# Kernel tuning notes

Hardware: AMD Instinct MI355X
Metric: run time of the kernel (lower is better)

The kernel has to match this reference:

```python
import jax, jax.numpy as jnp
import numpy as np

D = 256      # input channels
DK = 64      # key/query/value channels
BS, W, H = 8, 64, 64


def setup_inputs() -> dict:
    key = jax.random.key(0)
    k1, k2, k3, k4 = jax.random.split(key, 4)
    v = jax.random.normal(k1, (BS, D, W, H), dtype=jnp.float32)
    # conv1x1 weights collapse to plain matrices over the channel dim
    Wqkv = jax.random.normal(k2, (3 * DK, D), dtype=jnp.float32) * 0.02
    Wout = jax.random.normal(k3, (D, DK), dtype=jnp.float32) * 0.02
    gamma = jax.random.normal(k4, (1,), dtype=jnp.float32)  # original inits to 0; nonzero for a non-degenerate baseline
    return {"v": v, "Wqkv": Wqkv, "Wout": Wout, "gamma": gamma}


def reference(v, Wqkv, Wout, gamma):
    bs, c, w, h = v.shape
    n = w * h
    d_k = Wout.shape[1]
    x = v.reshape(bs, c, n)                      # (b, c, n)
    qkv = jnp.einsum('oc,bcn->bon', Wqkv, x)      # 1x1 conv == channel matmul
    q = qkv[:, :d_k]                              # (b, dk, n)
    k = qkv[:, d_k:2 * d_k]
    val = qkv[:, 2 * d_k:]
    s = jnp.einsum('bdi,bdj->bij', q, k)          # (b, n, n) = query^T key
    beta = jax.nn.softmax(s, axis=2)              # exp(s - logsumexp(s, axis=2))
    y = jnp.einsum('bdi,bij->bdj', val, beta)     # bmm(value, beta)
    o = jnp.einsum('od,bdn->bon', Wout, y) * gamma[0] + x
    return o.reshape(bs, c, w, h)
```

## Files before the change

### kernel.cpp

```cpp
#include <hip/hip_runtime.h>

typedef unsigned short ushort_t;
typedef __bf16 bf16x8 __attribute__((ext_vector_type(8)));
typedef short short4v __attribute__((ext_vector_type(4)));
typedef float f32x4 __attribute__((ext_vector_type(4)));
typedef unsigned int uint4v __attribute__((ext_vector_type(4)));
typedef unsigned int uint2v __attribute__((ext_vector_type(2)));

#define NTOK 4096
#define DMODEL 256
#define DK 64
#define BS 8
#define LN2INV 1.44269504088896f

__device__ __forceinline__ ushort_t f2bf(float f) {
  unsigned u = __builtin_bit_cast(unsigned, f);
  u += 0x7fffu + ((u >> 16) & 1u);
  return (ushort_t)(u >> 16);
}
__device__ __forceinline__ float bf2f(ushort_t s) {
  return __builtin_bit_cast(float, ((unsigned)s) << 16);
}
__device__ __forceinline__ bf16x8 lds_frag(const ushort_t* p) {
  return __builtin_bit_cast(bf16x8, *(const uint4v*)p);
}
__device__ __forceinline__ bf16x8 ldg8(const ushort_t* p) {
  return __builtin_bit_cast(bf16x8, *(const uint4v*)p);
}
__device__ __forceinline__ short4v lo8(uint4v v) {
  uint2v t; t.x = v.x; t.y = v.y;
  return __builtin_bit_cast(short4v, t);
}
__device__ __forceinline__ short4v hi8(uint4v v) {
  uint2v t; t.x = v.z; t.y = v.w;
  return __builtin_bit_cast(short4v, t);
}
__device__ __forceinline__ float fexp2(float x) {
#if __has_builtin(__builtin_amdgcn_exp2f)
  return __builtin_amdgcn_exp2f(x);
#else
  return exp2f(x);
#endif
}
__device__ __forceinline__ unsigned bfpack(float x, float y) {
  return __builtin_amdgcn_perm(__builtin_bit_cast(unsigned, y),
                               __builtin_bit_cast(unsigned, x), 0x07060302u);
}
__device__ __forceinline__ f32x4 mfma16(short4v a, short4v b, f32x4 c) {
#if defined(__HIP_DEVICE_COMPILE__)
#if __has_builtin(__builtin_amdgcn_mfma_f32_16x16x16bf16_1k)
  return __builtin_amdgcn_mfma_f32_16x16x16bf16_1k(a, b, c, 0, 0, 0);
#else
  typedef __bf16 bf16x4 __attribute__((ext_vector_type(4)));
  return __builtin_amdgcn_mfma_f32_16x16x16_bf16(__builtin_bit_cast(bf16x4, a),
                                                 __builtin_bit_cast(bf16x4, b), c, 0, 0, 0);
#endif
#else
  (void)a; (void)b;
  return c;
#endif
}

__global__ __launch_bounds__(256) void k_convert(const float* __restrict__ Wqkv,
                                                 const float* __restrict__ Wout,
                                                 ushort_t* __restrict__ Wb,
                                                 ushort_t* __restrict__ Woutb) {
  int i = blockIdx.x * 256 + threadIdx.x;
  if (i < 3 * DK * DMODEL) {
    float w = Wqkv[i];
    if (i < DK * DMODEL) w *= LN2INV;
    Wb[i] = f2bf(w);
  } else {
    int j = i - 3 * DK * DMODEL;
    Woutb[j] = f2bf(Wout[j]);
  }
}

__global__ __launch_bounds__(256) void k_qkv(const float* __restrict__ x,
                                             const ushort_t* __restrict__ W,
                                             ushort_t* __restrict__ QT,
                                             ushort_t* __restrict__ KT,
                                             ushort_t* __restrict__ Vf) {
  const int b = blockIdx.y;
  const int n0 = blockIdx.x * 64;
  const int tid = threadIdx.x;
  const int lane = tid & 63, wv = tid >> 6;
  const int quad = lane >> 4, l15 = lane & 15;
  __shared__ __align__(16) ushort_t lx[64 * 264];
  __shared__ __align__(16) ushort_t t[64 * 72];

  const float* xb = x + (size_t)b * DMODEL * NTOK;

#pragma unroll 1
  for (int cc = 0; cc < 4; cc++) {
    const int c0chunk = cc * 64;
#pragma unroll
    for (int kr = 0; kr < 2; kr++) {
      int s = tid + 256 * kr;
      int c = s >> 3, ns = (s & 7) * 8;
      const float* src = xb + (size_t)(c0chunk + c) * NTOK + n0 + ns;
      f32x4 a = *(const f32x4*)src;
      f32x4 bq = *(const f32x4*)(src + 4);
      uint4v o;
      o.x = (unsigned)f2bf(a[0]) | ((unsigned)f2bf(a[1]) << 16);
      o.y = (unsigned)f2bf(a[2]) | ((unsigned)f2bf(a[3]) << 16);
      o.z = (unsigned)f2bf(bq[0]) | ((unsigned)f2bf(bq[1]) << 16);
      o.w = (unsigned)f2bf(bq[2]) | ((unsigned)f2bf(bq[3]) << 16);
      *(uint4v*)(t + c * 72 + ns) = o;
    }
    __syncthreads();
#pragma unroll
    for (int kr = 0; kr < 2; kr++) {
      int s = tid + 256 * kr;
      int n = s >> 3, cs = (s & 7) * 8;
      unsigned e0 = t[(cs + 0) * 72 + n], e1 = t[(cs + 1) * 72 + n];
      unsigned e2 = t[(cs + 2) * 72 + n], e3 = t[(cs + 3) * 72 + n];
      unsigned e4 = t[(cs + 4) * 72 + n], e5 = t[(cs + 5) * 72 + n];
      unsigned e6 = t[(cs + 6) * 72 + n], e7 = t[(cs + 7) * 72 + n];
      uint4v o;
      o.x = e0 | (e1 << 16); o.y = e2 | (e3 << 16);
      o.z = e4 | (e5 << 16); o.w = e6 | (e7 << 16);
      *(uint4v*)(lx + n * 264 + c0chunk + cs) = o;
    }
    __syncthreads();
  }

  f32x4 acc[3][4];
  const f32x4 zero4 = {0.f, 0.f, 0.f, 0.f};
#pragma unroll
  for (int i = 0; i < 3; i++)
#pragma unroll
    for (int j = 0; j < 4; j++) acc[i][j] = zero4;

#pragma unroll
  for (int c0 = 0; c0 < DMODEL; c0 += 32) {
    bf16x8 aw[3];
#pragma unroll
    for (int mt = 0; mt < 3; mt++)
      aw[mt] = ldg8(W + (wv * 48 + mt * 16 + l15) * DMODEL + c0 + quad * 8);
    bf16x8 bb[4];
#pragma unroll
    for (int nt = 0; nt < 4; nt++)
      bb[nt] = lds_frag(lx + (nt * 16 + l15) * 264 + c0 + quad * 8);
#pragma unroll
    for (int mt = 0; mt < 3; mt++)
#pragma unroll
      for (int nt = 0; nt < 4; nt++)
        acc[mt][nt] = __builtin_amdgcn_mfma_f32_16x16x32_bf16(aw[mt], bb[nt], acc[mt][nt], 0, 0, 0);
  }

#pragma unroll
  for (int mt = 0; mt < 3; mt++) {
    int o = wv * 48 + mt * 16 + quad * 4;
#pragma unroll
    for (int nt = 0; nt < 4; nt++) {
      int n = n0 + nt * 16 + l15;
      f32x4 v4 = acc[mt][nt];
      if (o < 128) {
        ushort_t* dst = (o < 64) ? (QT + ((size_t)b * NTOK + n) * DK + o)
                                 : (KT + ((size_t)b * NTOK + n) * DK + (o - 64));
        uint2v ww;
        ww.x = (unsigned)f2bf(v4[0]) | ((unsigned)f2bf(v4[1]) << 16);
        ww.y = (unsigned)f2bf(v4[2]) | ((unsigned)f2bf(v4[3]) << 16);
        *(uint2v*)dst = ww;
      } else {
        int dbase = o - 128;
        size_t tbase = ((((size_t)b * 64 + (n0 >> 6)) * 4 + nt) * 2 + (dbase >> 5)) * 512;
        ushort_t* vp = Vf + tbase + ((l15 >> 2) << 7) + ((dbase & 15) << 3) +
                       (((dbase >> 4) & 1) << 2) + (l15 & 3);
#pragma unroll
        for (int r = 0; r < 4; r++) vp[r << 3] = f2bf(v4[r]);
      }
    }
  }
}

__global__ __launch_bounds__(512, 4) void k_rsum(const ushort_t* __restrict__ QT,
                                                 const ushort_t* __restrict__ KT,
                                                 float* __restrict__ Rr) {
  const int id = blockIdx.x;
  const int b = id & 7;
  const int i0 = (id >> 3) * 64;
  const int tid = threadIdx.x;
  const int lane = tid & 63, wv = tid >> 6;
  const int quad = lane >> 4, l15 = lane & 15;
  __shared__ __align__(16) float partial[8 * 64];
  const ushort_t* QTb = QT + ((size_t)b * NTOK + i0) * DK;
  const ushort_t* KTb = KT + ((size_t)b * NTOK + wv * 512) * DK;

  bf16x8 aq0[4], aq1[4];
#pragma unroll
  for (int isub = 0; isub < 4; isub++) {
    const ushort_t* qp = QTb + (size_t)(isub * 16 + l15) * DK + quad * 8;
    aq0[isub] = ldg8(qp);
    aq1[isub] = ldg8(qp + 32);
  }

  f32x4 racc[4];
  const f32x4 zero4 = {0.f, 0.f, 0.f, 0.f};
#pragma unroll
  for (int isub = 0; isub < 4; isub++) racc[isub] = zero4;

#pragma unroll 1
  for (int ph = 0; ph < 8; ph++) {
    const ushort_t* kb_base = KTb + (size_t)ph * 64 * DK;
    bf16x8 kb0[4], kb1[4];
#pragma unroll
    for (int nt = 0; nt < 4; nt++) {
      const ushort_t* kp = kb_base + (size_t)(nt * 16 + l15) * DK + quad * 8;
      kb0[nt] = ldg8(kp);
      kb1[nt] = ldg8(kp + 32);
    }
#pragma unroll
    for (int isub = 0; isub < 4; isub++)
#pragma unroll
      for (int nt = 0; nt < 4; nt++) {
        f32x4 s4 = __builtin_amdgcn_mfma_f32_16x16x32_bf16(aq0[isub], kb0[nt], zero4, 0, 0, 0);
        s4 = __builtin_amdgcn_mfma_f32_16x16x32_bf16(aq1[isub], kb1[nt], s4, 0, 0, 0);
        racc[isub][0] += fexp2(s4[0]);
        racc[isub][1] += fexp2(s4[1]);
        racc[isub][2] += fexp2(s4[2]);
        racc[isub][3] += fexp2(s4[3]);
      }
  }

#pragma unroll
  for (int isub = 0; isub < 4; isub++)
#pragma unroll
    for (int r = 0; r < 4; r++) {
      float v = racc[isub][r];
      v += __shfl_xor(v, 1);
      v += __shfl_xor(v, 2);
      v += __shfl_xor(v, 4);
      v += __shfl_xor(v, 8);
      racc[isub][r] = v;
    }
  if (l15 == 0) {
#pragma unroll
    for (int isub = 0; isub < 4; isub++)
      *(f32x4*)(partial + wv * 64 + isub * 16 + quad * 4) = racc[isub];
  }
  __syncthreads();
  if (tid < 64) {
    float s = 0.f;
#pragma unroll
    for (int w = 0; w < 8; w++) s += partial[w * 64 + tid];
    Rr[(size_t)b * NTOK + i0 + tid] = -__log2f(s);
  }
}

__global__ __launch_bounds__(256, 4) void k_pv(const ushort_t* __restrict__ QT,
                                               const ushort_t* __restrict__ KT,
                                               const ushort_t* __restrict__ Vf,
                                               const float* __restrict__ Rr,
                                               ushort_t* __restrict__ Yp) {
  const int id = blockIdx.x;
  const int b = id & 7;
  const int rest = id >> 3;
  const int j0 = (rest & 63) * 64;
  const int ih = rest >> 6;
  const int tid = threadIdx.x;
  const int lane = tid & 63, wv = tid >> 6;
  const int quad = lane >> 4, l15 = lane & 15;

  __shared__ __align__(16) ushort_t pool[13312];
  float* rbuf = (float*)pool;
  ushort_t* pbuf = pool + 8704;

  const ushort_t* KTb = KT + ((size_t)b * NTOK + j0) * DK;
  const ushort_t* QTb = QT + ((size_t)b * NTOK + ih * 2048) * DK;
  const ushort_t* Vfb = Vf + ((size_t)b * 64 + ih * 32) * 4096;
  const float* Rrb = Rr + (size_t)b * NTOK + ih * 2048;

  bf16x8 kb0[4], kb1[4];
#pragma unroll
  for (int nt = 0; nt < 4; nt++) {
    const ushort_t* kp = KTb + (size_t)(nt * 16 + l15) * DK + quad * 8;
    kb0[nt] = ldg8(kp);
    kb1[nt] = ldg8(kp + 32);
  }

  f32x4 yt[4][4];
  const f32x4 zero4 = {0.f, 0.f, 0.f, 0.f};
#pragma unroll
  for (int i = 0; i < 4; i++)
#pragma unroll
    for (int j = 0; j < 4; j++) yt[i][j] = zero4;

  const int qrow = (wv * 16 + l15) * DK + quad * 8;
  const int vfo = wv * 1024 + lane * 8;

#pragma unroll 1
  for (int it = 0; it < 32; it++) {
    const ushort_t* qp = QTb + (size_t)it * 64 * DK + qrow;
    bf16x8 a0 = ldg8(qp);
    bf16x8 a1 = ldg8(qp + 32);
    const ushort_t* vp = Vfb + (size_t)it * 4096 + vfo;
    uint4v vv0 = *(const uint4v*)vp;
    uint4v vv1 = *(const uint4v*)(vp + 512);
    f32x4 lrv = *(const f32x4*)(Rrb + it * 64 + wv * 16 + quad * 4);
    short4v vf0 = lo8(vv0), vf1 = hi8(vv0), vf2 = lo8(vv1), vf3 = hi8(vv1);
#pragma unroll
    for (int nt = 0; nt < 4; nt++) {
      f32x4 s4 = __builtin_amdgcn_mfma_f32_16x16x32_bf16(a0, kb0[nt], lrv, 0, 0, 0);
      s4 = __builtin_amdgcn_mfma_f32_16x16x32_bf16(a1, kb1[nt], s4, 0, 0, 0);
      uint2v wp;
      wp.x = bfpack(fexp2(s4[0]), fexp2(s4[1]));
      wp.y = bfpack(fexp2(s4[2]), fexp2(s4[3]));
      short4v wf = __builtin_bit_cast(short4v, wp);
      yt[nt][0] = mfma16(wf, vf0, yt[nt][0]);
      yt[nt][1] = mfma16(wf, vf1, yt[nt][1]);
      yt[nt][2] = mfma16(wf, vf2, yt[nt][2]);
      yt[nt][3] = mfma16(wf, vf3, yt[nt][3]);
    }
  }

  if (wv == 0) {
#pragma unroll
    for (int nt = 0; nt < 4; nt++)
#pragma unroll
      for (int dsub = 0; dsub < 4; dsub++)
        *(f32x4*)(rbuf + (dsub * 16 + l15) * 68 + nt * 16 + quad * 4) = yt[nt][dsub];
  }
  __syncthreads();
  if (wv == 1) {
#pragma unroll
    for (int nt = 0; nt < 4; nt++)
#pragma unroll
      for (int dsub = 0; dsub < 4; dsub++) {
        float* p = rbuf + (dsub * 16 + l15) * 68 + nt * 16 + quad * 4;
        *(f32x4*)p = *(const f32x4*)p + yt[nt][dsub];
      }
  }
  __syncthreads();
  if (wv == 2) {
#pragma unroll
    for (int nt = 0; nt < 4; nt++)
#pragma unroll
      for (int dsub = 0; dsub < 4; dsub++) {
        float* p = rbuf + (dsub * 16 + l15) * 68 + nt * 16 + quad * 4;
        *(f32x4*)p = *(const f32x4*)p + yt[nt][dsub];
      }
  }
  __syncthreads();
  if (wv == 3) {
#pragma unroll
    for (int nt = 0; nt < 4; nt++)
#pragma unroll
      for (int dsub = 0; dsub < 4; dsub++) {
        const float* p = rbuf + (dsub * 16 + l15) * 68 + nt * 16 + quad * 4;
        f32x4 v4 = *(const f32x4*)p + yt[nt][dsub];
#pragma unroll
        for (int r = 0; r < 4; r++)
          pbuf[(nt * 16 + quad * 4 + r) * 72 + dsub * 16 + l15] = f2bf(v4[r]);
      }
  }
  __syncthreads();

  ushort_t* Ypb = Yp + ((size_t)(ih * 8 + b) * NTOK + j0) * DK;
#pragma unroll
  for (int kr = 0; kr < 2; kr++) {
    int s = tid + 256 * kr;
    int row = s >> 3, cc = (s & 7) * 8;
    *(uint4v*)(Ypb + (size_t)row * DK + cc) = *(const uint4v*)(pbuf + row * 72 + cc);
  }
}

__global__ __launch_bounds__(256) void k_out(const ushort_t* __restrict__ Yp,
                                             const ushort_t* __restrict__ Wout,
                                             const float* __restrict__ gammap,
                                             const float* __restrict__ x,
                                             float* __restrict__ outp) {
  const int id = blockIdx.x;
  const int b = id & 7;
  const int n0 = (id >> 3) * 64;
  const int tid = threadIdx.x;
  const int lane = tid & 63, wv = tid >> 6;
  const int quad = lane >> 4, l15 = lane & 15;
  __shared__ __align__(16) ushort_t pbuf[64 * 72];

  const ushort_t* Y0 = Yp + ((size_t)b * NTOK + n0) * DK;
  const ushort_t* Y1 = Yp + ((size_t)(8 + b) * NTOK + n0) * DK;
#pragma unroll
  for (int kr = 0; kr < 2; kr++) {
    int s = tid + 256 * kr;
    int row = s >> 3, c8 = (s & 7) * 8;
    uint4v ua = *(const uint4v*)(Y0 + (size_t)row * DK + c8);
    uint4v ub = *(const uint4v*)(Y1 + (size_t)row * DK + c8);
    uint4v oc;
    unsigned* pa = (unsigned*)&ua;
    unsigned* pb = (unsigned*)&ub;
    unsigned* po = (unsigned*)&oc;
#pragma unroll
    for (int w = 0; w < 4; w++) {
      float lo = bf2f((ushort_t)(pa[w] & 0xffff)) + bf2f((ushort_t)(pb[w] & 0xffff));
      float hi = bf2f((ushort_t)(pa[w] >> 16)) + bf2f((ushort_t)(pb[w] >> 16));
      po[w] = bfpack(lo, hi);
    }
    *(uint4v*)(pbuf + row * 72 + c8) = oc;
  }
  __syncthreads();

  const f32x4 zero4 = {0.f, 0.f, 0.f, 0.f};
  bf16x8 yb0[4], yb1[4];
#pragma unroll
  for (int nt = 0; nt < 4; nt++) {
    yb0[nt] = lds_frag(pbuf + (nt * 16 + l15) * 72 + quad * 8);
    yb1[nt] = lds_frag(pbuf + (nt * 16 + l15) * 72 + 32 + quad * 8);
  }
  f32x4 oacc[4][4];
#pragma unroll
  for (int m = 0; m < 4; m++)
#pragma unroll
    for (int nt = 0; nt < 4; nt++) oacc[m][nt] = zero4;
#pragma unroll
  for (int m = 0; m < 4; m++) {
    int c = (wv * 4 + m) * 16 + l15;
    bf16x8 aw0 = __builtin_bit_cast(bf16x8, *(const uint4v*)(Wout + c * DK + quad * 8));
    bf16x8 aw1 = __builtin_bit_cast(bf16x8, *(const uint4v*)(Wout + c * DK + 32 + quad * 8));
#pragma unroll
    for (int nt = 0; nt < 4; nt++) {
      oacc[m][nt] = __builtin_amdgcn_mfma_f32_16x16x32_bf16(aw0, yb0[nt], oacc[m][nt], 0, 0, 0);
      oacc[m][nt] = __builtin_amdgcn_mfma_f32_16x16x32_bf16(aw1, yb1[nt], oacc[m][nt], 0, 0, 0);
    }
  }
  float g = gammap[0];
  const float* xb = x + (size_t)b * DMODEL * NTOK;
  float* ob = outp + (size_t)b * DMODEL * NTOK;
#pragma unroll
  for (int m = 0; m < 4; m++) {
    int cbase = (wv * 4 + m) * 16 + quad * 4;
#pragma unroll
    for (int nt = 0; nt < 4; nt++) {
      int n = n0 + nt * 16 + l15;
#pragma unroll
      for (int r = 0; r < 4; r++) {
        size_t idx = (size_t)(cbase + r) * NTOK + n;
        ob[idx] = oacc[m][nt][r] * g + xb[idx];
      }
    }
  }
}

extern "C" void kernel_launch(void* const* d_in, const int* in_sizes, int n_in,
                              void* d_out, int out_size, void* d_ws, size_t ws_size,
                              hipStream_t stream) {
  const float* v = (const float*)d_in[0];
  const float* Wqkv = (const float*)d_in[1];
  const float* Wout = (const float*)d_in[2];
  const float* gamma = (const float*)d_in[3];
  float* outp = (float*)d_out;

  ushort_t* QT = (ushort_t*)d_ws;
  ushort_t* KT = QT + (size_t)BS * NTOK * DK;
  ushort_t* Vf = KT + (size_t)BS * NTOK * DK;
  ushort_t* Wb = Vf + (size_t)BS * DK * NTOK;
  ushort_t* Woutb = Wb + 3 * DK * DMODEL;
  float* Rr = (float*)(Woutb + DMODEL * DK);
  ushort_t* Yp = (ushort_t*)(Rr + (size_t)BS * NTOK);

  k_convert<<<dim3(256), 256, 0, stream>>>(Wqkv, Wout, Wb, Woutb);
  k_qkv<<<dim3(64, BS), 256, 0, stream>>>(v, Wb, QT, KT, Vf);
  k_rsum<<<dim3(512), 512, 0, stream>>>(QT, KT, Rr);
  k_pv<<<dim3(1024), 256, 0, stream>>>(QT, KT, Vf, Rr, Yp);
  k_out<<<dim3(512), 256, 0, stream>>>(Yp, Woutb, gamma, v, outp);
}
```

Measured before the change: 203.9 us.

## Double-buffer Q and V tiles in k_pv via async global-to-LDS loads

```diff
diff --git a/kernel.cpp b/kernel.cpp
--- a/kernel.cpp
+++ b/kernel.cpp
@@ -58,6 +58,16 @@
 #else
   (void)a; (void)b;
   return c;
+#endif
+}
+
+typedef __attribute__((address_space(3))) unsigned int lds_u32;
+typedef const __attribute__((address_space(1))) unsigned int glob_u32;
+__device__ __forceinline__ void gll16(const void* g, void* l) {
+#if defined(__HIP_DEVICE_COMPILE__)
+  __builtin_amdgcn_global_load_lds((glob_u32*)g, (lds_u32*)l, 16, 0, 0);
+#else
+  (void)g; (void)l;
 #endif
 }
 
@@ -263,7 +273,9 @@
   const int lane = tid & 63, wv = tid >> 6;
   const int quad = lane >> 4, l15 = lane & 15;
 
-  __shared__ __align__(16) ushort_t pool[13312];
+  __shared__ __align__(16) ushort_t pool[20480];
+  float* lrtab = (float*)pool;
+  ushort_t* wbuf = pool + 4096 + wv * 4096;
   float* rbuf = (float*)pool;
   ushort_t* pbuf = pool + 8704;
 
@@ -272,6 +284,21 @@
   const ushort_t* Vfb = Vf + ((size_t)b * 64 + ih * 32) * 4096;
   const float* Rrb = Rr + (size_t)b * NTOK + ih * 2048;
 
+  const int qrow = (wv * 16 + l15) * DK + quad * 8;
+  const int vfo = wv * 1024 + lane * 8;
+
+  gll16(QTb + qrow,       wbuf);
+  gll16(QTb + qrow + 32,  wbuf + 512);
+  gll16(Vfb + vfo,        wbuf + 1024);
+  gll16(Vfb + vfo + 512,  wbuf + 1536);
+
+  {
+    f32x4 r0 = *(const f32x4*)(Rrb + tid * 8);
+    f32x4 r1 = *(const f32x4*)(Rrb + tid * 8 + 4);
+    *(f32x4*)(lrtab + tid * 8) = r0;
+    *(f32x4*)(lrtab + tid * 8 + 4) = r1;
+  }
+
   bf16x8 kb0[4], kb1[4];
 #pragma unroll
   for (int nt = 0; nt < 4; nt++) {
@@ -280,6 +307,8 @@
     kb1[nt] = ldg8(kp + 32);
   }
 
+  __syncthreads();
+
   f32x4 yt[4][4];
   const f32x4 zero4 = {0.f, 0.f, 0.f, 0.f};
 #pragma unroll
@@ -287,18 +316,27 @@
 #pragma unroll
     for (int j = 0; j < 4; j++) yt[i][j] = zero4;
 
-  const int qrow = (wv * 16 + l15) * DK + quad * 8;
-  const int vfo = wv * 1024 + lane * 8;
-
 #pragma unroll 1
   for (int it = 0; it < 32; it++) {
-    const ushort_t* qp = QTb + (size_t)it * 64 * DK + qrow;
-    bf16x8 a0 = ldg8(qp);
-    bf16x8 a1 = ldg8(qp + 32);
-    const ushort_t* vp = Vfb + (size_t)it * 4096 + vfo;
-    uint4v vv0 = *(const uint4v*)vp;
-    uint4v vv1 = *(const uint4v*)(vp + 512);
-    f32x4 lrv = *(const f32x4*)(Rrb + it * 64 + wv * 16 + quad * 4);
+    const int cb = it & 1, nb = cb ^ 1;
+    const int tpre = (it + 1 < 32) ? it + 1 : 31;
+    {
+      const ushort_t* qp = QTb + (size_t)tpre * 64 * DK + qrow;
+      const ushort_t* vp = Vfb + (size_t)tpre * 4096 + vfo;
+      ushort_t* nbuf = wbuf + nb * 2048;
+      gll16(qp,       nbuf);
+      gll16(qp + 32,  nbuf + 512);
+      gll16(vp,       nbuf + 1024);
+      gll16(vp + 512, nbuf + 1536);
+    }
+    asm volatile("s_waitcnt vmcnt(4)" ::: "memory");
+    __builtin_amdgcn_sched_barrier(0);
+    const ushort_t* cbuf = wbuf + cb * 2048;
+    bf16x8 a0 = lds_frag(cbuf + lane * 8);
+    bf16x8 a1 = lds_frag(cbuf + 512 + lane * 8);
+    uint4v vv0 = *(const uint4v*)(cbuf + 1024 + lane * 8);
+    uint4v vv1 = *(const uint4v*)(cbuf + 1536 + lane * 8);
+    f32x4 lrv = *(const f32x4*)(lrtab + it * 64 + wv * 16 + quad * 4);
     short4v vf0 = lo8(vv0), vf1 = hi8(vv0), vf2 = lo8(vv1), vf3 = hi8(vv1);
 #pragma unroll
     for (int nt = 0; nt < 4; nt++) {
@@ -314,6 +352,9 @@
       yt[nt][3] = mfma16(wf, vf3, yt[nt][3]);
     }
   }
+
+  asm volatile("s_waitcnt vmcnt(0)" ::: "memory");
+  __syncthreads();
 
   if (wv == 0) {
 #pragma unroll
```

Measured after the change: 201.9 us. About the same (-1.0%).
